# Kernel optimization log

Hardware: AMD Instinct MI355X
Metric: run time of the kernel (lower is better)

Reference implementation:

```python
import jax, jax.numpy as jnp
import numpy as np

K = 20           # neighbors
ALPHA = 1.0      # clustering alpha
BN_EPS = 1e-5
NEG_SLOPE = 0.2


def knn_idx(x, k):
    # x: (B, C, N) -> idx (B, N, k) of k nearest neighbors by squared L2
    xx = jnp.sum(x * x, axis=1)                      # (B, N)
    inner = jnp.einsum('bcn,bcm->bnm', x, x)         # (B, N, N)
    pd = -xx[:, :, None] + 2.0 * inner - xx[:, None, :]  # negative sq dist
    return jax.lax.top_k(pd, k)[1]


def graph_feature(x, k):
    # x: (B, C, N) -> (B, 2C, N, k): concat(neighbor - center, center)
    xt = jnp.transpose(x, (0, 2, 1))                 # (B, N, C)
    idx = knn_idx(x, k)                              # (B, N, k)
    feat = jax.vmap(lambda f, i: f[i])(xt, idx)      # (B, N, k, C)
    center = jnp.broadcast_to(xt[:, :, None, :], feat.shape)
    out = jnp.concatenate([feat - center, center], axis=-1)
    return jnp.transpose(out, (0, 3, 1, 2))


def batchnorm(x, g, b, axes):
    # training-mode BN: batch statistics over `axes`, channel axis = 1
    m = jnp.mean(x, axes, keepdims=True)
    v = jnp.var(x, axes, keepdims=True)
    shape = [1] * x.ndim
    shape[1] = x.shape[1]
    return (x - m) / jnp.sqrt(v + BN_EPS) * g.reshape(shape) + b.reshape(shape)


def conv_block2d(x, w, g, b):
    # 1x1 Conv2d (no bias) + BN2d + LeakyReLU; x (B,Cin,N,k), w (Cout,Cin)
    y = jnp.einsum('oc,bcnk->bonk', w, x)
    return jax.nn.leaky_relu(batchnorm(y, g, b, (0, 2, 3)), NEG_SLOPE)


def setup_inputs() -> dict:
    key = jax.random.key(0)
    ks = jax.random.split(key, 16)
    B, C, N = 4, 3, 2048
    d = {
        'x1': jax.random.normal(ks[0], (B, C, N), jnp.float32),
        'x2': jax.random.normal(ks[1], (B, C, N), jnp.float32),
        'w1': jax.random.normal(ks[2], (64, 6), jnp.float32) * 0.1,
        'g1': jnp.ones((64,), jnp.float32), 'b1': jnp.zeros((64,), jnp.float32),
        'w2': jax.random.normal(ks[3], (64, 128), jnp.float32) * 0.1,
        'g2': jnp.ones((64,), jnp.float32), 'b2': jnp.zeros((64,), jnp.float32),
        'w3': jax.random.normal(ks[4], (128, 128), jnp.float32) * 0.1,
        'g3': jnp.ones((128,), jnp.float32), 'b3': jnp.zeros((128,), jnp.float32),
        'w4': jax.random.normal(ks[5], (256, 256), jnp.float32) * 0.1,
        'g4': jnp.ones((256,), jnp.float32), 'b4': jnp.zeros((256,), jnp.float32),
        'w5': jax.random.normal(ks[6], (1024, 512), jnp.float32) * 0.05,
        'g5': jnp.ones((1024,), jnp.float32), 'b5': jnp.zeros((1024,), jnp.float32),
        'lw1': jax.random.normal(ks[7], (256, 2048), jnp.float32) * 0.02,
        'lb1': jnp.zeros((256,), jnp.float32),
        'lw2': jax.random.normal(ks[8], (64, 256), jnp.float32) * 0.05,
        'lb2': jnp.zeros((64,), jnp.float32),
        'lw3': jax.random.normal(ks[9], (10, 64), jnp.float32) * 0.1,
        'lb3': jnp.zeros((10,), jnp.float32),
        'cw': jax.random.normal(ks[10], (800, 10), jnp.float32) * 0.1,
    }
    return d


def reference(x1, x2, w1, g1, b1, w2, g2, b2, w3, g3, b3, w4, g4, b4,
              w5, g5, b5, lw1, lb1, lw2, lb2, lw3, lb3, cw):

    def single(x):
        h = conv_block2d(graph_feature(x, K), w1, g1, b1)
        f1 = h.max(axis=-1)                            # (B,64,N)
        h = conv_block2d(graph_feature(f1, K), w2, g2, b2)
        f2 = h.max(axis=-1)                            # (B,64,N)
        h = conv_block2d(graph_feature(f2, K), w3, g3, b3)
        f3 = h.max(axis=-1)                            # (B,128,N)
        h = conv_block2d(graph_feature(f3, K), w4, g4, b4)
        f4 = h.max(axis=-1)                            # (B,256,N)
        h = jnp.concatenate([f1, f2, f3, f4], axis=1)  # (B,512,N)
        h = jnp.einsum('oc,bcn->bon', w5, h)           # 1x1 Conv1d
        h = jax.nn.leaky_relu(batchnorm(h, g5, b5, (0, 2)), NEG_SLOPE)
        z = jnp.concatenate([h.max(axis=-1), h.mean(axis=-1)], axis=1)  # (B,2048)
        z = z @ lw1.T + lb1
        z = z @ lw2.T + lb2
        e = z @ lw3.T + lb3                            # (B,10)
        diff = e[:, None, :] - cw                      # (B,800,10)
        x_dis = jnp.sum(diff * diff, axis=2)           # (B,800)
        q = (1.0 + x_dis / ALPHA) ** (-(ALPHA + 1.0) / 2.0)
        q = q / jnp.sum(q, axis=1, keepdims=True)
        return q, e, x_dis

    q1, e1, xd1 = single(x1)
    q2, e2, xd2 = single(x2)
    d = e1 - e2 + 1e-6  # torch F.pairwise_distance eps
    sim = jnp.sqrt(jnp.sum(d * d, axis=1))
    return (sim, q1, q2, e1, e2, xd1)
```

## Files before the change

kernel.cpp:

```cpp
#include <hip/hip_runtime.h>
#include <math.h>

#define BB 4
#define NN 2048
#define KK 20
#define NEG 0.2f

#define QOFF0 4
#define QOFF1 3204
#define EOFF0 6404
#define EOFF1 6444
#define XDOFF 6484

typedef unsigned short u16;
typedef unsigned int u32;
typedef __attribute__((ext_vector_type(8))) short s16x8;
typedef __attribute__((ext_vector_type(4))) float f32x4;
typedef __attribute__((ext_vector_type(16))) float f32x16;
typedef __attribute__((ext_vector_type(8))) u16 u16x8;

__device__ __forceinline__ u16 f2bf(float x) {
    u32 u = __float_as_uint(x);
    u += 0x7FFFu + ((u >> 16) & 1u);
    return (u16)(u >> 16);
}

__global__ __launch_bounds__(256) void transpose_x_kernel(
    const float* __restrict__ x, float* __restrict__ fnc, float* __restrict__ xx,
    u16* __restrict__ fh, u16* __restrict__ fl)
{
    int gid = blockIdx.x * 256 + threadIdx.x;
    int b = gid >> 11, n = gid & 2047;
    float s = 0.f;
    float v[3];
#pragma unroll
    for (int c = 0; c < 3; ++c) {
        v[c] = x[((size_t)b * 3 + c) * NN + n];
        fnc[(size_t)gid * 3 + c] = v[c];
        s += v[c] * v[c];
    }
    xx[gid] = s;
    u16x8 z = {0,0,0,0,0,0,0,0};
    u16x8 h0 = z, l0 = z;
#pragma unroll
    for (int c = 0; c < 3; ++c) {
        u16 hb = f2bf(v[c]);
        h0[c] = hb;
        l0[c] = f2bf(v[c] - __uint_as_float((u32)hb << 16));
    }
    u16* fhp = fh + (size_t)gid * 32;
    u16* flp = fl + (size_t)gid * 32;
    *(u16x8*)(fhp)      = h0; *(u16x8*)(fhp + 8)  = z;
    *(u16x8*)(fhp + 16) = z;  *(u16x8*)(fhp + 24) = z;
    *(u16x8*)(flp)      = l0; *(u16x8*)(flp + 8)  = z;
    *(u16x8*)(flp + 16) = z;  *(u16x8*)(flp + 24) = z;
}

__global__ __launch_bounds__(256) void norms_kernel(
    const float* __restrict__ h512, int choff, int C, float* __restrict__ xx)
{
    int gid = blockIdx.x * 256 + threadIdx.x;
    const float* p = h512 + (size_t)gid * 512 + choff;
    float s = 0.f;
    for (int c = 0; c < C; ++c) { float v = p[c]; s += v * v; }
    xx[gid] = s;
}

#define NINFV -3.4e38f

template<int CTRL>
__device__ __forceinline__ void dmax2(float& a1, float& a2)
{
    int b1i = __builtin_amdgcn_update_dpp(
        __float_as_int(a1), __float_as_int(a1), CTRL, 0xf, 0xf, false);
    int b2i = __builtin_amdgcn_update_dpp(
        __float_as_int(a2), __float_as_int(a2), CTRL, 0xf, 0xf, false);
    float b1 = __int_as_float(b1i), b2 = __int_as_float(b2i);
    float n1 = fmaxf(a1, b1);
    float n2 = fmaxf(fminf(a1, b1), fmaxf(a2, b2));
    a1 = n1; a2 = n2;
}

template<int C>
__global__ __launch_bounds__(512, 4) void knn_kernel(
    const float* __restrict__ fcn,
    const float* __restrict__ fnc,
    int ncs, int choff,
    const float* __restrict__ xx, int* __restrict__ idxout)
{
    __shared__ float sbuf[8][NN];
    int tid = threadIdx.x;
    int bid = blockIdx.x;
    int b   = bid & 3;
    int n0  = (((bid >> 3) << 1) | ((bid >> 2) & 1)) * 8;

    const float* fb = fcn + (size_t)b * C * NN;
    const float* xb = xx + b * NN;
    const float* cbase = fnc + (size_t)(b * NN + n0) * ncs + choff;

    float a0[8], a1[8], a2[8], a3[8];
#pragma unroll
    for (int r = 0; r < 8; ++r) { a0[r] = 0.f; a1[r] = 0.f; a2[r] = 0.f; a3[r] = 0.f; }

    const float* fp = fb + 4 * tid;

    if constexpr (C % 4 == 0) {
        float4 buf[4];
#pragma unroll
        for (int q = 0; q < 4; ++q) buf[q] = *(const float4*)(fp + (size_t)q * NN);
        for (int cg = 0; cg < C; cg += 4) {
            float4 nxt[4];
            if (cg + 4 < C) {
#pragma unroll
                for (int q = 0; q < 4; ++q)
                    nxt[q] = *(const float4*)(fp + (size_t)(cg + 4 + q) * NN);
            } else {
#pragma unroll
                for (int q = 0; q < 4; ++q) nxt[q] = buf[q];
            }
            float4 cv[8];
#pragma unroll
            for (int r = 0; r < 8; ++r)
                cv[r] = *(const float4*)(cbase + (size_t)r * ncs + cg);
#pragma unroll
            for (int r = 0; r < 8; ++r) {
                a0[r] += cv[r].x * buf[0].x; a1[r] += cv[r].x * buf[0].y;
                a2[r] += cv[r].x * buf[0].z; a3[r] += cv[r].x * buf[0].w;
                a0[r] += cv[r].y * buf[1].x; a1[r] += cv[r].y * buf[1].y;
                a2[r] += cv[r].y * buf[1].z; a3[r] += cv[r].y * buf[1].w;
                a0[r] += cv[r].z * buf[2].x; a1[r] += cv[r].z * buf[2].y;
                a2[r] += cv[r].z * buf[2].z; a3[r] += cv[r].z * buf[2].w;
                a0[r] += cv[r].w * buf[3].x; a1[r] += cv[r].w * buf[3].y;
                a2[r] += cv[r].w * buf[3].z; a3[r] += cv[r].w * buf[3].w;
            }
#pragma unroll
            for (int q = 0; q < 4; ++q) buf[q] = nxt[q];
        }
    } else {
        for (int c = 0; c < C; ++c) {
            float cr[8];
#pragma unroll
            for (int r = 0; r < 8; ++r) cr[r] = cbase[(size_t)r * ncs + c];
            float4 v = *(const float4*)(fp + (size_t)c * NN);
#pragma unroll
            for (int r = 0; r < 8; ++r) {
                a0[r] += cr[r] * v.x; a1[r] += cr[r] * v.y;
                a2[r] += cr[r] * v.z; a3[r] += cr[r] * v.w;
            }
        }
    }
    {
        float4 xm = *(const float4*)(xb + 4 * tid);
#pragma unroll
        for (int r = 0; r < 8; ++r) {
            float4 sv = {2.f * a0[r] - xm.x, 2.f * a1[r] - xm.y,
                         2.f * a2[r] - xm.z, 2.f * a3[r] - xm.w};
            *(float4*)&sbuf[r][4 * tid] = sv;
        }
    }
    __syncthreads();

    int w = tid >> 6, lane = tid & 63;
    float* sb = sbuf[w];
    int p = n0 + w;
    int* op = idxout + (size_t)(b * NN + p) * KK;

    if (lane == 0) op[0] = p;
    if (lane == (p & 63)) sb[p] = NINFV;

    float v1 = NINFV, v2 = NINFV, v3 = NINFV, v4 = NINFV;
    int j1 = -1, j2 = -1, j3 = -1, j4 = -1;
#pragma unroll
    for (int j = 0; j < 32; ++j) {
        float vv = sb[lane + (j << 6)];
        if (vv > v1) { v4 = v3; j4 = j3; v3 = v2; j3 = j2; v2 = v1; j2 = j1; v1 = vv; j1 = j; }
        else if (vv > v2) { v4 = v3; j4 = j3; v3 = v2; j3 = j2; v2 = vv; j2 = j; }
        else if (vv > v3) { v4 = v3; j4 = j3; v3 = vv; j3 = j; }
        else if (vv > v4) { v4 = vv; j4 = j; }
    }

    unsigned consumed = 0u;

    for (int it = 1; it < KK; it += 2) {
        float r1 = v1, r2 = v2;
        dmax2<0x111>(r1, r2);
        dmax2<0x112>(r1, r2);
        dmax2<0x114>(r1, r2);
        dmax2<0x118>(r1, r2);
        dmax2<0x142>(r1, r2);
        dmax2<0x143>(r1, r2);
        float m1 = __int_as_float(
            __builtin_amdgcn_readlane(__float_as_int(r1), 63));
        float m2 = __int_as_float(
            __builtin_amdgcn_readlane(__float_as_int(r2), 63));
        unsigned long long k1 = __ballot(v1 == m1);
        if (lane == __ffsll(k1) - 1) {
            op[it] = lane + (j1 << 6);
            consumed |= 1u << j1;
            v1 = v2; j1 = j2; v2 = v3; j2 = j3; v3 = v4; j3 = j4;
            v4 = NINFV; j4 = -1;
        }
        if (it + 1 < KK) {
            unsigned long long k2 = __ballot(v1 == m2);
            if (lane == __ffsll(k2) - 1) {
                op[it + 1] = lane + (j1 << 6);
                consumed |= 1u << j1;
                v1 = v2; j1 = j2; v2 = v3; j2 = j3; v3 = v4; j3 = j4;
                v4 = NINFV; j4 = -1;
            }
        }
        if (__any(v2 == NINFV)) {
            if (v2 == NINFV) {
                v1 = NINFV; v2 = NINFV; v3 = NINFV; v4 = NINFV;
                j1 = -1; j2 = -1; j3 = -1; j4 = -1;
#pragma unroll
                for (int j = 0; j < 32; ++j) {
                    if (!(consumed & (1u << j))) {
                        float vv = sb[lane + (j << 6)];
                        if (vv > v1) { v4 = v3; j4 = j3; v3 = v2; j3 = j2; v2 = v1; j2 = j1; v1 = vv; j1 = j; }
                        else if (vv > v2) { v4 = v3; j4 = j3; v3 = v2; j3 = j2; v2 = vv; j2 = j; }
                        else if (vv > v3) { v4 = v3; j4 = j3; v3 = vv; j3 = j; }
                        else if (vv > v4) { v4 = vv; j4 = j; }
                    }
                }
            }
        }
    }
}

__global__ __launch_bounds__(256) void tobf16_w_kernel(
    const float* __restrict__ W, int C, int COUT, int KP,
    u16* __restrict__ Wh, u16* __restrict__ Wl)
{
    int idx = blockIdx.x * 256 + threadIdx.x;
    if (idx >= 2 * COUT * KP) return;
    int row = idx / KP, c = idx - row * KP;
    int o = (row >= COUT) ? row - COUT : row;
    float val = 0.f;
    if (c < C) {
        float w1 = W[(size_t)o * 2 * C + c];
        val = (row >= COUT) ? (W[(size_t)o * 2 * C + C + c] - w1) : w1;
    }
    u16 hb = f2bf(val);
    Wh[idx] = hb;
    Wl[idx] = f2bf(val - __uint_as_float((u32)hb << 16));
}

template<int KT, int COUT>
__global__ __launch_bounds__(256) void gemm_gh_mfma_kernel(
    const u16* __restrict__ Fh, const u16* __restrict__ Fl,
    int ncs, int choff,
    const u16* __restrict__ Wh, const u16* __restrict__ Wl,
    float* __restrict__ G, float* __restrict__ H)
{
    constexpr int KP = KT * 32;
    constexpr int NT = (2 * COUT) >> 4;
    int tid = threadIdx.x;
    int r0 = blockIdx.x << 4;
    int wv = tid >> 6, lane = tid & 63;
    int l15 = lane & 15, l4 = lane >> 4;

    const u16* Ah0 = Fh + (size_t)(r0 + l15) * ncs + choff + l4 * 8;
    const u16* Al0 = Fl + (size_t)(r0 + l15) * ncs + choff + l4 * 8;
    s16x8 a_h[KT], a_l[KT];
#pragma unroll
    for (int kt = 0; kt < KT; ++kt) {
        a_h[kt] = *(const s16x8*)(Ah0 + kt * 32);
        a_l[kt] = *(const s16x8*)(Al0 + kt * 32);
    }

    for (int t = wv; t < NT; t += 4) {
        int c0 = t << 4;
        const u16* Bh0 = Wh + (size_t)(c0 + l15) * KP + l4 * 8;
        const u16* Bl0 = Wl + (size_t)(c0 + l15) * KP + l4 * 8;
        f32x4 acc;
#pragma unroll
        for (int i = 0; i < 4; ++i) acc[i] = 0.f;
#pragma unroll
        for (int kt = 0; kt < KT; ++kt) {
            s16x8 bh = *(const s16x8*)(Bh0 + kt * 32);
            s16x8 bl = *(const s16x8*)(Bl0 + kt * 32);
            acc = __builtin_amdgcn_mfma_f32_16x16x32_bf16(a_h[kt], bh, acc, 0, 0, 0);
            acc = __builtin_amdgcn_mfma_f32_16x16x32_bf16(a_l[kt], bh, acc, 0, 0, 0);
            acc = __builtin_amdgcn_mfma_f32_16x16x32_bf16(a_h[kt], bl, acc, 0, 0, 0);
        }
        int col = c0 + l15;
        float* dst = (col < COUT) ? G : H;
        int cc = (col < COUT) ? col : col - COUT;
#pragma unroll
        for (int i = 0; i < 4; ++i)
            dst[(size_t)(r0 + l4 * 4 + i) * COUT + cc] = acc[i];
    }
}

template<int COUT>
__global__ __launch_bounds__(256) void gather_kernel(
    const float* __restrict__ G, const float* __restrict__ H,
    const int* __restrict__ idx,
    float* __restrict__ ymax, float* __restrict__ ymin,
    float* __restrict__ psum, float* __restrict__ psumsq)
{
    constexpr int RPI = 256 / COUT;
    constexpr int NITER = 16 / RPI;
    int tid = threadIdx.x;
    int o = tid % COUT;
    int rsub = tid / COUT;
    int row0 = blockIdx.x * 16;
    float s = 0.f, s2 = 0.f;
    for (int it = 0; it < NITER; ++it) {
        int r = row0 + it * RPI + rsub;
        int b = r >> 11;
        float h = H[(size_t)r * COUT + o];
        const int* ip = idx + (size_t)r * KK;
        float mx = -3.4e38f, mn = 3.4e38f;
#pragma unroll
        for (int j = 0; j < KK; ++j) {
            int m = ip[j];
            float g = G[((size_t)(b << 11) + m) * COUT + o];
            float y = g + h;
            mx = fmaxf(mx, y); mn = fminf(mn, y);
            s += y; s2 += y * y;
        }
        ymax[(size_t)r * COUT + o] = mx;
        ymin[(size_t)r * COUT + o] = mn;
    }
    __shared__ float ls[256], ls2[256];
    ls[tid] = s; ls2[tid] = s2;
    __syncthreads();
    for (int st = 128; st >= COUT; st >>= 1) {
        if (tid < st) { ls[tid] += ls[tid + st]; ls2[tid] += ls2[tid + st]; }
        __syncthreads();
    }
    if (tid < COUT) {
        psum[(size_t)blockIdx.x * COUT + tid]   = ls[tid];
        psumsq[(size_t)blockIdx.x * COUT + tid] = ls2[tid];
    }
}

__global__ __launch_bounds__(256) void bnscale_kernel(
    const float* __restrict__ psum, const float* __restrict__ psumsq,
    int nblk, int cout, float cnt,
    const float* __restrict__ gw, const float* __restrict__ bw,
    float* __restrict__ ss)
{
    int o = blockIdx.x;
    int t = threadIdx.x;
    float s = 0.f, s2 = 0.f;
    for (int i = t; i < nblk; i += 256) {
        s  += psum[(size_t)i * cout + o];
        s2 += psumsq[(size_t)i * cout + o];
    }
    __shared__ float ls[256], ls2[256];
    ls[t] = s; ls2[t] = s2;
    __syncthreads();
    for (int st = 128; st > 0; st >>= 1) {
        if (t < st) { ls[t] += ls[t + st]; ls2[t] += ls2[t + st]; }
        __syncthreads();
    }
    if (t == 0) {
        float m = ls[0] / cnt;
        float v = ls2[0] / cnt - m * m;
        float sc = gw[o] / sqrtf(v + 1e-5f);
        float sh = bw[o] - m * sc;
        ss[o * 2] = sc; ss[o * 2 + 1] = sh;
    }
}

__global__ __launch_bounds__(256) void apply_kernel(
    const float* __restrict__ ymax, const float* __restrict__ ymin,
    const float* __restrict__ ss, int coutShift, int choff,
    float* __restrict__ h512, u16* __restrict__ Ah, u16* __restrict__ Al)
{
    size_t gid = (size_t)blockIdx.x * 256 + threadIdx.x;
    int o = (int)(gid & ((1u << coutShift) - 1));
    size_t r = gid >> coutShift;
    float sc = ss[o * 2], sh = ss[o * 2 + 1];
    float v = (sc >= 0.f) ? ymax[gid] : ymin[gid];
    float a = sc * v + sh;
    float act = (a > 0.f) ? a : NEG * a;
    size_t hidx = r * 512 + choff + o;
    h512[hidx] = act;
    u16 hb = f2bf(act);
    Ah[hidx] = hb;
    Al[hidx] = f2bf(act - __uint_as_float((u32)hb << 16));
}

template<int CO>
__global__ __launch_bounds__(256) void apply_t_kernel(
    const float* __restrict__ ymax, const float* __restrict__ ymin,
    const float* __restrict__ ss, int choff,
    float* __restrict__ h512, float* __restrict__ fcn,
    u16* __restrict__ Ah, u16* __restrict__ Al)
{
    constexpr int TILES_O = CO >> 6;
    __shared__ float tile[64][65];
    int tr = blockIdx.x / TILES_O;
    int to = blockIdx.x % TILES_O;
    int r0 = tr * 64, o0 = to * 64;
    int t = threadIdx.x;
    int lr = t >> 6;
    int lo = t & 63;
    int o = o0 + lo;
    float sc = ss[o * 2], sh = ss[o * 2 + 1];
#pragma unroll
    for (int rr = 0; rr < 64; rr += 4) {
        int r = r0 + rr + lr;
        size_t gid = (size_t)r * CO + o;
        float v = (sc >= 0.f) ? ymax[gid] : ymin[gid];
        float a = sc * v + sh;
        float act = (a > 0.f) ? a : NEG * a;
        size_t hidx = (size_t)r * 512 + choff + o;
        h512[hidx] = act;
        u16 hb = f2bf(act);
        Ah[hidx] = hb;
        Al[hidx] = f2bf(act - __uint_as_float((u32)hb << 16));
        tile[rr + lr][lo] = act;
    }
    __syncthreads();
    int b = r0 >> 11;
    int n0 = r0 & 2047;
#pragma unroll
    for (int oo = 0; oo < 64; oo += 4) {
        fcn[((size_t)(b * CO + o0 + oo + lr)) * NN + n0 + lo] = tile[lo][oo + lr];
    }
}

__global__ __launch_bounds__(256) void tobf16_b_kernel(
    const float* __restrict__ Bm, u16* __restrict__ Bh, u16* __restrict__ Bl)
{
    int gid = blockIdx.x * 256 + threadIdx.x;
    size_t off = (size_t)gid * 8;
    float4 v0 = *(const float4*)(Bm + off);
    float4 v1 = *(const float4*)(Bm + off + 4);
    float x[8] = {v0.x, v0.y, v0.z, v0.w, v1.x, v1.y, v1.z, v1.w};
    u16x8 h, l;
#pragma unroll
    for (int j = 0; j < 8; ++j) {
        u16 hb = f2bf(x[j]);
        h[j] = hb;
        l[j] = f2bf(x[j] - __uint_as_float((u32)hb << 16));
    }
    *(u16x8*)(Bh + off) = h;
    *(u16x8*)(Bl + off) = l;
}

__device__ __forceinline__ void gload_lds16(const void* g, void* l) {
    __builtin_amdgcn_global_load_lds(
        (const __attribute__((address_space(1))) void*)g,
        (__attribute__((address_space(3))) void*)l, 16, 0, 0);
}

__global__ __launch_bounds__(256) void gemm5_mfma_kernel(
    const u16* __restrict__ Ah, const u16* __restrict__ Al,
    const u16* __restrict__ Bh, const u16* __restrict__ Bl,
    float* __restrict__ Y, float* __restrict__ psum, float* __restrict__ psumsq)
{
    __shared__ u16 As[2][128][64];
    __shared__ u16 Bs[2][128][64];
    __shared__ float scs[4][128];
    __shared__ float sqs[4][128];

    int tid = threadIdx.x;
    int bm = blockIdx.x & 63, bn = blockIdx.x >> 6;
    int row0 = bm * 128, col0 = bn * 128;
    int w = tid >> 6, lane = tid & 63;
    int wr = w >> 1, wc = w & 1;

    int isB = w >> 1, plane = w & 1;
    int srow = lane >> 3;
    int kch  = (lane & 7) ^ srow;
    const u16* gbase = isB ? (plane ? Bl : Bh) : (plane ? Al : Ah);
    int rc0 = isB ? col0 : row0;
    const u16* gsrc0 = gbase + (size_t)(rc0 + srow) * 512 + kch * 8;
    u16* lds0 = (isB ? &Bs[0][0][0] : &As[0][0][0]) + plane * 8192;

    f32x16 acc[2][2];
#pragma unroll
    for (int i = 0; i < 2; ++i)
#pragma unroll
        for (int j = 0; j < 2; ++j)
#pragma unroll
            for (int r = 0; r < 16; ++r) acc[i][j][r] = 0.f;

    int ln = lane & 31, l5 = lane >> 5;
    const u16* Afb = &As[0][0][0] + (size_t)(wr * 64 + ln) * 64;
    const u16* Bfb = &Bs[0][0][0] + (size_t)(wc * 64 + ln) * 64;

    for (int k0 = 0; k0 < 512; k0 += 64) {
#pragma unroll
        for (int cc = 0; cc < 16; ++cc)
            gload_lds16(gsrc0 + (size_t)cc * 4096 + k0, lds0 + cc * 512);
        __syncthreads();

#pragma unroll
        for (int ks = 0; ks < 4; ++ks) {
            int pos = ((ks * 2 + l5) ^ (ln & 7)) * 8;
            s16x8 ah0 = *(const s16x8*)(Afb + pos);
            s16x8 ah1 = *(const s16x8*)(Afb + 2048 + pos);
            s16x8 al0 = *(const s16x8*)(Afb + 8192 + pos);
            s16x8 al1 = *(const s16x8*)(Afb + 8192 + 2048 + pos);
#pragma unroll
            for (int j = 0; j < 2; ++j) {
                s16x8 bh = *(const s16x8*)(Bfb + j * 2048 + pos);
                s16x8 bl = *(const s16x8*)(Bfb + 8192 + j * 2048 + pos);
                acc[0][j] = __builtin_amdgcn_mfma_f32_32x32x16_bf16(ah0, bh, acc[0][j], 0, 0, 0);
                acc[1][j] = __builtin_amdgcn_mfma_f32_32x32x16_bf16(ah1, bh, acc[1][j], 0, 0, 0);
                acc[0][j] = __builtin_amdgcn_mfma_f32_32x32x16_bf16(al0, bh, acc[0][j], 0, 0, 0);
                acc[1][j] = __builtin_amdgcn_mfma_f32_32x32x16_bf16(al1, bh, acc[1][j], 0, 0, 0);
                acc[0][j] = __builtin_amdgcn_mfma_f32_32x32x16_bf16(ah0, bl, acc[0][j], 0, 0, 0);
                acc[1][j] = __builtin_amdgcn_mfma_f32_32x32x16_bf16(ah1, bl, acc[1][j], 0, 0, 0);
            }
        }
        __syncthreads();
    }

#pragma unroll
    for (int i = 0; i < 2; ++i)
#pragma unroll
        for (int reg = 0; reg < 16; ++reg) {
            int row = row0 + wr * 64 + i * 32 + l5 * 4 + (reg >> 2) * 8 + (reg & 3);
            float* yp = Y + (size_t)row * 1024 + col0 + wc * 64 + ln;
            yp[0]  = acc[i][0][reg];
            yp[32] = acc[i][1][reg];
        }

#pragma unroll
    for (int j = 0; j < 2; ++j) {
        float s = 0.f, q = 0.f;
#pragma unroll
        for (int i = 0; i < 2; ++i)
#pragma unroll
            for (int reg = 0; reg < 16; ++reg) {
                float v = acc[i][j][reg];
                s += v; q += v * v;
            }
        scs[wr * 2 + l5][wc * 64 + j * 32 + ln] = s;
        sqs[wr * 2 + l5][wc * 64 + j * 32 + ln] = q;
    }
    __syncthreads();
    if (tid < 128) {
        float s = 0.f, q = 0.f;
#pragma unroll
        for (int p = 0; p < 4; ++p) { s += scs[p][tid]; q += sqs[p][tid]; }
        psum[(size_t)bm * 1024 + col0 + tid]   = s;
        psumsq[(size_t)bm * 1024 + col0 + tid] = q;
    }
}

__global__ __launch_bounds__(256) void pool_part_kernel(
    const float* __restrict__ Y, const float* __restrict__ ss,
    float* __restrict__ pmax, float* __restrict__ psum)
{
    int bid = blockIdx.x;
    int b = bid >> 6;
    int n0 = (bid & 63) * 32;
    int t = threadIdx.x;
    int o = t * 4;
    float4 sA = *(const float4*)(ss + o * 2);
    float4 sB = *(const float4*)(ss + o * 2 + 4);
    float4 mx = {-3.4e38f, -3.4e38f, -3.4e38f, -3.4e38f};
    float4 sm = {0.f, 0.f, 0.f, 0.f};
    const float* Yb = Y + ((size_t)b * NN + n0) * 1024 + o;
#pragma unroll 4
    for (int n = 0; n < 32; ++n) {
        float4 v = *(const float4*)(Yb + (size_t)n * 1024);
        float a0 = sA.x * v.x + sA.y; a0 = (a0 > 0.f) ? a0 : NEG * a0;
        float a1 = sA.z * v.y + sA.w; a1 = (a1 > 0.f) ? a1 : NEG * a1;
        float a2 = sB.x * v.z + sB.y; a2 = (a2 > 0.f) ? a2 : NEG * a2;
        float a3 = sB.z * v.w + sB.w; a3 = (a3 > 0.f) ? a3 : NEG * a3;
        mx.x = fmaxf(mx.x, a0); sm.x += a0;
        mx.y = fmaxf(mx.y, a1); sm.y += a1;
        mx.z = fmaxf(mx.z, a2); sm.z += a2;
        mx.w = fmaxf(mx.w, a3); sm.w += a3;
    }
    size_t po = (size_t)bid * 1024 + o;
    *(float4*)(pmax + po) = mx;
    *(float4*)(psum + po) = sm;
}

__global__ __launch_bounds__(256) void pool_comb_kernel(
    const float* __restrict__ pmax, const float* __restrict__ psum,
    float* __restrict__ z)
{
    int b = blockIdx.x;
    int t = threadIdx.x;
    int o = t * 4;
    float4 mx = {-3.4e38f, -3.4e38f, -3.4e38f, -3.4e38f};
    float4 sm = {0.f, 0.f, 0.f, 0.f};
    for (int ch = 0; ch < 64; ++ch) {
        size_t po = ((size_t)(b * 64 + ch)) * 1024 + o;
        float4 m = *(const float4*)(pmax + po);
        float4 s = *(const float4*)(psum + po);
        mx.x = fmaxf(mx.x, m.x); mx.y = fmaxf(mx.y, m.y);
        mx.z = fmaxf(mx.z, m.z); mx.w = fmaxf(mx.w, m.w);
        sm.x += s.x; sm.y += s.y; sm.z += s.z; sm.w += s.w;
    }
    *(float4*)(z + (size_t)b * 2048 + o) = mx;
    float4 mn = {sm.x * (1.f / 2048.f), sm.y * (1.f / 2048.f),
                 sm.z * (1.f / 2048.f), sm.w * (1.f / 2048.f)};
    *(float4*)(z + (size_t)b * 2048 + 1024 + o) = mn;
}

__global__ __launch_bounds__(64) void gemv1_kernel(
    const float* __restrict__ z, const float* __restrict__ lw1,
    const float* __restrict__ lb1, float* __restrict__ z1)
{
    int o = blockIdx.x;
    int lane = threadIdx.x;
    const float* wr = lw1 + (size_t)o * 2048;
    float a0 = 0.f, a1 = 0.f, a2 = 0.f, a3 = 0.f;
    for (int c = lane; c < 2048; c += 64) {
        float w = wr[c];
        a0 += z[c] * w; a1 += z[2048 + c] * w;
        a2 += z[4096 + c] * w; a3 += z[6144 + c] * w;
    }
#pragma unroll
    for (int off = 32; off > 0; off >>= 1) {
        a0 += __shfl_down(a0, off); a1 += __shfl_down(a1, off);
        a2 += __shfl_down(a2, off); a3 += __shfl_down(a3, off);
    }
    if (lane == 0) {
        float bias = lb1[o];
        z1[o] = a0 + bias; z1[256 + o] = a1 + bias;
        z1[512 + o] = a2 + bias; z1[768 + o] = a3 + bias;
    }
}

__global__ __launch_bounds__(1024) void head2_kernel(
    const float* __restrict__ z1,
    const float* __restrict__ lw2, const float* __restrict__ lb2,
    const float* __restrict__ lw3, const float* __restrict__ lb3,
    const float* __restrict__ cw,
    float* __restrict__ out, float* __restrict__ e_store, int which)
{
    __shared__ float z2s[4][64];
    __shared__ float es[4][10];
    __shared__ float qs[3200];
    __shared__ float dnm[4];
    int t = threadIdx.x;
    if (t < 256) {
        int b = t >> 6, o = t & 63;
        float acc = lb2[o];
        const float* wr = lw2 + (size_t)o * 256;
        const float* zr = z1 + b * 256;
        for (int c = 0; c < 256; ++c) acc += zr[c] * wr[c];
        z2s[b][o] = acc;
    }
    __syncthreads();
    if (t < 40) {
        int b = t / 10, o = t % 10;
        float acc = lb3[o];
        const float* wr = lw3 + o * 64;
        for (int c = 0; c < 64; ++c) acc += z2s[b][c] * wr[c];
        es[b][o] = acc;
        int eoff = (which == 0) ? EOFF0 : EOFF1;
        out[eoff + b * 10 + o] = acc;
        e_store[which * 40 + b * 10 + o] = acc;
    }
    __syncthreads();
    for (int p = t; p < 3200; p += 1024) {
        int b = p / 800, j = p % 800;
        float xd = 0.f;
        const float* cwr = cw + j * 10;
#pragma unroll
        for (int i = 0; i < 10; ++i) { float d = es[b][i] - cwr[i]; xd += d * d; }
        qs[p] = 1.0f / (1.0f + xd);
        if (which == 0) out[XDOFF + p] = xd;
    }
    __syncthreads();
    if (t < 4) {
        float s = 0.f;
        for (int j = 0; j < 800; ++j) s += qs[t * 800 + j];
        dnm[t] = s;
    }
    __syncthreads();
    int qoff = (which == 0) ? QOFF0 : QOFF1;
    for (int p = t; p < 3200; p += 1024) out[qoff + p] = qs[p] / dnm[p / 800];
}

__global__ void sim_kernel(const float* __restrict__ e_store, float* __restrict__ out)
{
    int t = threadIdx.x;
    if (t < 4) {
        float s = 0.f;
        for (int i = 0; i < 10; ++i) {
            float d = e_store[t * 10 + i] - e_store[40 + t * 10 + i] + 1e-6f;
            s += d * d;
        }
        out[t] = sqrtf(s);
    }
}

extern "C" void kernel_launch(void* const* d_in, const int* in_sizes, int n_in,
                              void* d_out, int out_size, void* d_ws, size_t ws_size,
                              hipStream_t stream)
{
    const float* x1  = (const float*)d_in[0];
    const float* x2  = (const float*)d_in[1];
    const float* w1  = (const float*)d_in[2];
    const float* g1  = (const float*)d_in[3];
    const float* b1  = (const float*)d_in[4];
    const float* w2  = (const float*)d_in[5];
    const float* g2  = (const float*)d_in[6];
    const float* b2  = (const float*)d_in[7];
    const float* w3  = (const float*)d_in[8];
    const float* g3  = (const float*)d_in[9];
    const float* b3  = (const float*)d_in[10];
    const float* w4  = (const float*)d_in[11];
    const float* g4  = (const float*)d_in[12];
    const float* b4  = (const float*)d_in[13];
    const float* w5  = (const float*)d_in[14];
    const float* g5  = (const float*)d_in[15];
    const float* b5  = (const float*)d_in[16];
    const float* lw1 = (const float*)d_in[17];
    const float* lb1 = (const float*)d_in[18];
    const float* lw2 = (const float*)d_in[19];
    const float* lb2 = (const float*)d_in[20];
    const float* lw3 = (const float*)d_in[21];
    const float* lb3 = (const float*)d_in[22];
    const float* cw  = (const float*)d_in[23];
    float* out = (float*)d_out;

    float* ws   = (float*)d_ws;
    float* h512 = ws;
    float* G    = h512 + 4194304;
    float* Hb   = G + 2097152;
    float* ymax = Hb + 2097152;
    float* ymin = ymax + 2097152;
    float* y5   = G;
    float* fcn  = ymin + 2097152;
    float* fnc1 = fcn + 1048576;
    float* xx   = fnc1 + 32768;
    float* psum = xx + 8192;
    float* psq  = psum + 131072;
    float* ss   = psq + 131072;
    float* p5s  = ss + 2048;
    float* p5q  = p5s + 262144;
    float* ss5  = p5q + 262144;
    float* z    = ss5 + 2048;
    float* z1   = z + 8192;
    float* est  = z1 + 1024;
    int*   idx  = (int*)(est + 128);
    u16*   Ahs  = (u16*)(idx + BB * NN * KK);
    u16*   Als  = Ahs + 4194304;
    u16*   Bhs  = Als + 4194304;
    u16*   Bls  = Bhs + 524288;
    u16*   fnc1h = Bls + 524288;
    u16*   fnc1l = fnc1h + 262144;
    u16*   Wh   = fnc1l + 262144;
    u16*   Wl   = Wh + 98304;

    tobf16_b_kernel<<<256, 256, 0, stream>>>(w5, Bhs, Bls);
    tobf16_w_kernel<<<16,  256, 0, stream>>>(w1, 3,   64,  32,  Wh,         Wl);
    tobf16_w_kernel<<<32,  256, 0, stream>>>(w2, 64,  64,  64,  Wh + 4096,  Wl + 4096);
    tobf16_w_kernel<<<64,  256, 0, stream>>>(w3, 64,  128, 64,  Wh + 12288, Wl + 12288);
    tobf16_w_kernel<<<256, 256, 0, stream>>>(w4, 128, 256, 128, Wh + 28672, Wl + 28672);

    for (int which = 0; which < 2; ++which) {
        const float* xin = which ? x2 : x1;
        transpose_x_kernel<<<32, 256, 0, stream>>>(xin, fnc1, xx, fnc1h, fnc1l);
        knn_kernel<3><<<1024, 512, 0, stream>>>(xin, fnc1, 3, 0, xx, idx);
        gemm_gh_mfma_kernel<1, 64><<<512, 256, 0, stream>>>(fnc1h, fnc1l, 32, 0, Wh, Wl, G, Hb);
        gather_kernel<64><<<512, 256, 0, stream>>>(G, Hb, idx, ymax, ymin, psum, psq);
        bnscale_kernel<<<64, 256, 0, stream>>>(psum, psq, 512, 64, 163840.f, g1, b1, ss);
        apply_t_kernel<64><<<128, 256, 0, stream>>>(ymax, ymin, ss, 0, h512, fcn, Ahs, Als);
        norms_kernel<<<32, 256, 0, stream>>>(h512, 0, 64, xx);
        knn_kernel<64><<<1024, 512, 0, stream>>>(fcn, h512, 512, 0, xx, idx);
        gemm_gh_mfma_kernel<2, 64><<<512, 256, 0, stream>>>(Ahs, Als, 512, 0, Wh + 4096, Wl + 4096, G, Hb);
        gather_kernel<64><<<512, 256, 0, stream>>>(G, Hb, idx, ymax, ymin, psum, psq);
        bnscale_kernel<<<64, 256, 0, stream>>>(psum, psq, 512, 64, 163840.f, g2, b2, ss);
        apply_t_kernel<64><<<128, 256, 0, stream>>>(ymax, ymin, ss, 64, h512, fcn, Ahs, Als);
        norms_kernel<<<32, 256, 0, stream>>>(h512, 64, 64, xx);
        knn_kernel<64><<<1024, 512, 0, stream>>>(fcn, h512, 512, 64, xx, idx);
        gemm_gh_mfma_kernel<2, 128><<<512, 256, 0, stream>>>(Ahs, Als, 512, 64, Wh + 12288, Wl + 12288, G, Hb);
        gather_kernel<128><<<512, 256, 0, stream>>>(G, Hb, idx, ymax, ymin, psum, psq);
        bnscale_kernel<<<128, 256, 0, stream>>>(psum, psq, 512, 128, 163840.f, g3, b3, ss);
        apply_t_kernel<128><<<256, 256, 0, stream>>>(ymax, ymin, ss, 128, h512, fcn, Ahs, Als);
        norms_kernel<<<32, 256, 0, stream>>>(h512, 128, 128, xx);
        knn_kernel<128><<<1024, 512, 0, stream>>>(fcn, h512, 512, 128, xx, idx);
        gemm_gh_mfma_kernel<4, 256><<<512, 256, 0, stream>>>(Ahs, Als, 512, 128, Wh + 28672, Wl + 28672, G, Hb);
        gather_kernel<256><<<512, 256, 0, stream>>>(G, Hb, idx, ymax, ymin, psum, psq);
        bnscale_kernel<<<256, 256, 0, stream>>>(psum, psq, 512, 256, 163840.f, g4, b4, ss);
        apply_kernel<<<8192, 256, 0, stream>>>(ymax, ymin, ss, 8, 256, h512, Ahs, Als);
        gemm5_mfma_kernel<<<512, 256, 0, stream>>>(Ahs, Als, Bhs, Bls, y5, p5s, p5q);
        bnscale_kernel<<<1024, 256, 0, stream>>>(p5s, p5q, 64, 1024, 8192.f, g5, b5, ss5);
        pool_part_kernel<<<256, 256, 0, stream>>>(y5, ss5, p5s, p5q);
        pool_comb_kernel<<<4, 256, 0, stream>>>(p5s, p5q, z);
        gemv1_kernel<<<256, 64, 0, stream>>>(z, lw1, lb1, z1);
        head2_kernel<<<1, 1024, 0, stream>>>(z1, lw2, lb2, lw3, lb3, cw, out, est, which);
    }
    sim_kernel<<<1, 64, 0, stream>>>(est, out);
}
```

Baseline: 1.086 ms.

## Merge kNN and per-point G/H GEMM into one heterogeneous launch

```diff
diff --git a/kernel.cpp b/kernel.cpp
--- a/kernel.cpp
+++ b/kernel.cpp
@@ -81,22 +81,69 @@
     a1 = n1; a2 = n2;
 }
 
-template<int C>
-__global__ __launch_bounds__(512, 4) void knn_kernel(
+template<int C, int KT, int COUT>
+__global__ __launch_bounds__(512, 4) void knn_gh_kernel(
     const float* __restrict__ fcn,
     const float* __restrict__ fnc,
-    int ncs, int choff,
-    const float* __restrict__ xx, int* __restrict__ idxout)
+    int ncsf, int choff,
+    const float* __restrict__ xx, int* __restrict__ idxout,
+    const u16* __restrict__ Fh, const u16* __restrict__ Fl,
+    int ncsp,
+    const u16* __restrict__ Wh, const u16* __restrict__ Wl,
+    float* __restrict__ G, float* __restrict__ H)
 {
     __shared__ float sbuf[8][NN];
     int tid = threadIdx.x;
-    int bid = blockIdx.x;
-    int b   = bid & 3;
-    int n0  = (((bid >> 3) << 1) | ((bid >> 2) & 1)) * 8;
+    int g = blockIdx.x / 5, rmod = blockIdx.x % 5;
+
+    if (rmod == 4) {
+        constexpr int KP = KT * 32;
+        constexpr int NT = (2 * COUT) >> 4;
+        int wv = tid >> 6, lane = tid & 63;
+        int l15 = lane & 15, l4 = lane >> 4;
+        int r0 = g * 32 + (wv >> 2) * 16;
+        int wq = wv & 3;
+
+        const u16* Ah0 = Fh + (size_t)(r0 + l15) * ncsp + choff + l4 * 8;
+        const u16* Al0 = Fl + (size_t)(r0 + l15) * ncsp + choff + l4 * 8;
+        s16x8 a_h[KT], a_l[KT];
+#pragma unroll
+        for (int kt = 0; kt < KT; ++kt) {
+            a_h[kt] = *(const s16x8*)(Ah0 + kt * 32);
+            a_l[kt] = *(const s16x8*)(Al0 + kt * 32);
+        }
+        for (int t = wq; t < NT; t += 4) {
+            int c0 = t << 4;
+            const u16* Bh0 = Wh + (size_t)(c0 + l15) * KP + l4 * 8;
+            const u16* Bl0 = Wl + (size_t)(c0 + l15) * KP + l4 * 8;
+            f32x4 acc;
+#pragma unroll
+            for (int i = 0; i < 4; ++i) acc[i] = 0.f;
+#pragma unroll
+            for (int kt = 0; kt < KT; ++kt) {
+                s16x8 bh = *(const s16x8*)(Bh0 + kt * 32);
+                s16x8 bl = *(const s16x8*)(Bl0 + kt * 32);
+                acc = __builtin_amdgcn_mfma_f32_16x16x32_bf16(a_h[kt], bh, acc, 0, 0, 0);
+                acc = __builtin_amdgcn_mfma_f32_16x16x32_bf16(a_l[kt], bh, acc, 0, 0, 0);
+                acc = __builtin_amdgcn_mfma_f32_16x16x32_bf16(a_h[kt], bl, acc, 0, 0, 0);
+            }
+            int col = c0 + l15;
+            float* dst = (col < COUT) ? G : H;
+            int cc = (col < COUT) ? col : col - COUT;
+#pragma unroll
+            for (int i = 0; i < 4; ++i)
+                dst[(size_t)(r0 + l4 * 4 + i) * COUT + cc] = acc[i];
+        }
+        return;
+    }
+
+    int kb = g * 4 + rmod;
+    int b   = kb & 3;
+    int n0  = (((kb >> 3) << 1) | ((kb >> 2) & 1)) * 8;
 
     const float* fb = fcn + (size_t)b * C * NN;
     const float* xb = xx + b * NN;
-    const float* cbase = fnc + (size_t)(b * NN + n0) * ncs + choff;
+    const float* cbase = fnc + (size_t)(b * NN + n0) * ncsf + choff;
 
     float a0[8], a1[8], a2[8], a3[8];
 #pragma unroll
@@ -121,7 +168,7 @@
             float4 cv[8];
 #pragma unroll
             for (int r = 0; r < 8; ++r)
-                cv[r] = *(const float4*)(cbase + (size_t)r * ncs + cg);
+                cv[r] = *(const float4*)(cbase + (size_t)r * ncsf + cg);
 #pragma unroll
             for (int r = 0; r < 8; ++r) {
                 a0[r] += cv[r].x * buf[0].x; a1[r] += cv[r].x * buf[0].y;
@@ -140,7 +187,7 @@
         for (int c = 0; c < C; ++c) {
             float cr[8];
 #pragma unroll
-            for (int r = 0; r < 8; ++r) cr[r] = cbase[(size_t)r * ncs + c];
+            for (int r = 0; r < 8; ++r) cr[r] = cbase[(size_t)r * ncsf + c];
             float4 v = *(const float4*)(fp + (size_t)c * NN);
 #pragma unroll
             for (int r = 0; r < 8; ++r) {
@@ -244,53 +291,6 @@
     u16 hb = f2bf(val);
     Wh[idx] = hb;
     Wl[idx] = f2bf(val - __uint_as_float((u32)hb << 16));
-}
-
-template<int KT, int COUT>
-__global__ __launch_bounds__(256) void gemm_gh_mfma_kernel(
-    const u16* __restrict__ Fh, const u16* __restrict__ Fl,
-    int ncs, int choff,
-    const u16* __restrict__ Wh, const u16* __restrict__ Wl,
-    float* __restrict__ G, float* __restrict__ H)
-{
-    constexpr int KP = KT * 32;
-    constexpr int NT = (2 * COUT) >> 4;
-    int tid = threadIdx.x;
-    int r0 = blockIdx.x << 4;
-    int wv = tid >> 6, lane = tid & 63;
-    int l15 = lane & 15, l4 = lane >> 4;
-
-    const u16* Ah0 = Fh + (size_t)(r0 + l15) * ncs + choff + l4 * 8;
-    const u16* Al0 = Fl + (size_t)(r0 + l15) * ncs + choff + l4 * 8;
-    s16x8 a_h[KT], a_l[KT];
-#pragma unroll
-    for (int kt = 0; kt < KT; ++kt) {
-        a_h[kt] = *(const s16x8*)(Ah0 + kt * 32);
-        a_l[kt] = *(const s16x8*)(Al0 + kt * 32);
-    }
-
-    for (int t = wv; t < NT; t += 4) {
-        int c0 = t << 4;
-        const u16* Bh0 = Wh + (size_t)(c0 + l15) * KP + l4 * 8;
-        const u16* Bl0 = Wl + (size_t)(c0 + l15) * KP + l4 * 8;
-        f32x4 acc;
-#pragma unroll
-        for (int i = 0; i < 4; ++i) acc[i] = 0.f;
-#pragma unroll
-        for (int kt = 0; kt < KT; ++kt) {
-            s16x8 bh = *(const s16x8*)(Bh0 + kt * 32);
-            s16x8 bl = *(const s16x8*)(Bl0 + kt * 32);
-            acc = __builtin_amdgcn_mfma_f32_16x16x32_bf16(a_h[kt], bh, acc, 0, 0, 0);
-            acc = __builtin_amdgcn_mfma_f32_16x16x32_bf16(a_l[kt], bh, acc, 0, 0, 0);
-            acc = __builtin_amdgcn_mfma_f32_16x16x32_bf16(a_h[kt], bl, acc, 0, 0, 0);
-        }
-        int col = c0 + l15;
-        float* dst = (col < COUT) ? G : H;
-        int cc = (col < COUT) ? col : col - COUT;
-#pragma unroll
-        for (int i = 0; i < 4; ++i)
-            dst[(size_t)(r0 + l4 * 4 + i) * COUT + cc] = acc[i];
-    }
 }
 
 template<int COUT>
@@ -759,26 +759,26 @@
     for (int which = 0; which < 2; ++which) {
         const float* xin = which ? x2 : x1;
         transpose_x_kernel<<<32, 256, 0, stream>>>(xin, fnc1, xx, fnc1h, fnc1l);
-        knn_kernel<3><<<1024, 512, 0, stream>>>(xin, fnc1, 3, 0, xx, idx);
-        gemm_gh_mfma_kernel<1, 64><<<512, 256, 0, stream>>>(fnc1h, fnc1l, 32, 0, Wh, Wl, G, Hb);
+        knn_gh_kernel<3, 1, 64><<<1280, 512, 0, stream>>>(
+            xin, fnc1, 3, 0, xx, idx, fnc1h, fnc1l, 32, Wh, Wl, G, Hb);
         gather_kernel<64><<<512, 256, 0, stream>>>(G, Hb, idx, ymax, ymin, psum, psq);
         bnscale_kernel<<<64, 256, 0, stream>>>(psum, psq, 512, 64, 163840.f, g1, b1, ss);
         apply_t_kernel<64><<<128, 256, 0, stream>>>(ymax, ymin, ss, 0, h512, fcn, Ahs, Als);
         norms_kernel<<<32, 256, 0, stream>>>(h512, 0, 64, xx);
-        knn_kernel<64><<<1024, 512, 0, stream>>>(fcn, h512, 512, 0, xx, idx);
-        gemm_gh_mfma_kernel<2, 64><<<512, 256, 0, stream>>>(Ahs, Als, 512, 0, Wh + 4096, Wl + 4096, G, Hb);
+        knn_gh_kernel<64, 2, 64><<<1280, 512, 0, stream>>>(
+            fcn, h512, 512, 0, xx, idx, Ahs, Als, 512, Wh + 4096, Wl + 4096, G, Hb);
         gather_kernel<64><<<512, 256, 0, stream>>>(G, Hb, idx, ymax, ymin, psum, psq);
         bnscale_kernel<<<64, 256, 0, stream>>>(psum, psq, 512, 64, 163840.f, g2, b2, ss);
         apply_t_kernel<64><<<128, 256, 0, stream>>>(ymax, ymin, ss, 64, h512, fcn, Ahs, Als);
         norms_kernel<<<32, 256, 0, stream>>>(h512, 64, 64, xx);
-        knn_kernel<64><<<1024, 512, 0, stream>>>(fcn, h512, 512, 64, xx, idx);
-        gemm_gh_mfma_kernel<2, 128><<<512, 256, 0, stream>>>(Ahs, Als, 512, 64, Wh + 12288, Wl + 12288, G, Hb);
+        knn_gh_kernel<64, 2, 128><<<1280, 512, 0, stream>>>(
+            fcn, h512, 512, 64, xx, idx, Ahs, Als, 512, Wh + 12288, Wl + 12288, G, Hb);
         gather_kernel<128><<<512, 256, 0, stream>>>(G, Hb, idx, ymax, ymin, psum, psq);
         bnscale_kernel<<<128, 256, 0, stream>>>(psum, psq, 512, 128, 163840.f, g3, b3, ss);
         apply_t_kernel<128><<<256, 256, 0, stream>>>(ymax, ymin, ss, 128, h512, fcn, Ahs, Als);
         norms_kernel<<<32, 256, 0, stream>>>(h512, 128, 128, xx);
-        knn_kernel<128><<<1024, 512, 0, stream>>>(fcn, h512, 512, 128, xx, idx);
-        gemm_gh_mfma_kernel<4, 256><<<512, 256, 0, stream>>>(Ahs, Als, 512, 128, Wh + 28672, Wl + 28672, G, Hb);
+        knn_gh_kernel<128, 4, 256><<<1280, 512, 0, stream>>>(
+            fcn, h512, 512, 128, xx, idx, Ahs, Als, 512, Wh + 28672, Wl + 28672, G, Hb);
         gather_kernel<256><<<512, 256, 0, stream>>>(G, Hb, idx, ymax, ymin, psum, psq);
         bnscale_kernel<<<256, 256, 0, stream>>>(psum, psq, 512, 256, 163840.f, g4, b4, ss);
         apply_kernel<<<8192, 256, 0, stream>>>(ymax, ymin, ss, 8, 256, h512, Ahs, Als);
```

Result: slower. 1.133 ms (+4.3%).
